# Optimization experiments

Hardware: AMD Instinct MI355X
Metric: run time of the kernel (lower is better)

The kernel has to match this reference:

```python
import jax, jax.numpy as jnp
import numpy as np

IN_SIZES = [64, 128, 256]
HIDDEN = [512, 512]
ENC = 256
COUNTS = [100000, 80000, 60000]


def _xavier(key, fan_in, fan_out):
    # xavier_uniform with gain('sigmoid') == 1
    lim = float(np.sqrt(6.0 / (fan_in + fan_out)))
    return jax.random.uniform(key, (fan_in, fan_out), jnp.float32, -lim, lim)


def setup_inputs() -> dict:
    key = jax.random.key(0)
    ks = jax.random.split(key, 32)
    inp = {}
    ki = 0
    for t, (n, d) in enumerate(zip(COUNTS, IN_SIZES)):
        inp[f"x{t}"] = jax.random.normal(ks[ki], (n, d), dtype=jnp.float32)
        ki += 1
    # node_type sorted by type, counts match x tensors (invariant of the module)
    inp["node_type"] = jnp.concatenate(
        [jnp.full((n,), t, dtype=jnp.int32) for t, n in enumerate(COUNTS)])
    for t, d_in in enumerate(IN_SIZES):
        sizes = [d_in] + HIDDEN + [ENC]
        for i in range(len(sizes) - 1):
            inp[f"W{t}_{i+1}"] = _xavier(ks[ki], sizes[i], sizes[i + 1])
            ki += 1
            inp[f"b{t}_{i+1}"] = jnp.zeros((sizes[i + 1],), jnp.float32)
    return inp


def _mlp(x, layers):
    # each layer is Linear followed by Sigmoid (including the last)
    for W, b in layers:
        x = jax.nn.sigmoid(x @ W + b)
    return x


def reference(x0, x1, x2, node_type,
              W0_1, b0_1, W0_2, b0_2, W0_3, b0_3,
              W1_1, b1_1, W1_2, b1_2, W1_3, b1_3,
              W2_1, b2_1, W2_2, b2_2, W2_3, b2_3):
    xs = [x0, x1, x2]
    params = [
        [(W0_1, b0_1), (W0_2, b0_2), (W0_3, b0_3)],
        [(W1_1, b1_1), (W1_2, b1_2), (W1_3, b1_3)],
        [(W2_1, b2_1), (W2_2, b2_2), (W2_3, b2_3)],
    ]
    N = node_type.shape[0]
    X = jnp.zeros((N, ENC), dtype=jnp.float32)
    for nt in range(len(xs)):
        # static per-type count -> fixed-size nonzero works under jit
        idx = jnp.nonzero(node_type == nt, size=xs[nt].shape[0])[0]
        X = X.at[idx].set(_mlp(xs[nt], params[nt]))
    return X
```

## Files before the change

### kernel.cpp

```cpp
#include <hip/hip_runtime.h>
#include <hip/hip_bf16.h>

typedef __bf16 bf16x8 __attribute__((ext_vector_type(8)));
typedef __bf16 bf16x4 __attribute__((ext_vector_type(4)));
typedef float  f32x16 __attribute__((ext_vector_type(16)));

#define BM 64
#define S  520
#define SF 260

struct PrepParams {
    const float* src[9];
    int Kt[9];
    int Mg[9];
    int N[9];
    int blkEnd[9];
    int unitBase[9];
};

__global__ void __launch_bounds__(256)
prep_weights(PrepParams p, uint4* __restrict__ dst) {
    __shared__ float tile[32][128];
    int b = blockIdx.x;
    int w = 0;
    while (b >= p.blkEnd[w]) ++w;
    int local = b - ((w == 0) ? 0 : p.blkEnd[w - 1]);
    int mgc = p.Mg[w];
    int kt = local / mgc;
    int mg = local - kt * mgc;
    const float* src = p.src[w];
    int N = p.N[w];
    int Kc = p.Kt[w] * 2;
    int t = threadIdx.x;

    int row0 = kt * 32, col0 = mg * 128;
#pragma unroll
    for (int i = 0; i < 4; ++i) {
        int e4 = t + i * 256;
        int r = e4 >> 5;
        int c4 = e4 & 31;
        float4 v = *(const float4*)&src[(size_t)(row0 + r) * N + col0 + c4 * 4];
        *(float4*)&tile[r][c4 * 4] = v;
    }
    __syncthreads();

#pragma unroll
    for (int rep = 0; rep < 2; ++rep) {
        int ul = t + rep * 256;
        int lane = ul & 63;
        int kcl = (ul >> 6) & 1;
        int mtl = ul >> 7;
        int gUnit = p.unitBase[w] +
                    ((mg * 4 + mtl) * Kc + (kt * 2 + kcl)) * 64 + lane;
        int lr = kcl * 16 + ((lane >> 5) << 3);
        int lc = mtl * 32 + (lane & 31);
        alignas(16) unsigned short u8[8];
#pragma unroll
        for (int j = 0; j < 8; ++j)
            u8[j] = __builtin_bit_cast(unsigned short, (__bf16)tile[lr + j][lc]);
        dst[gUnit] = *(const uint4*)u8;
    }
}

struct MlpParams {
    const float* X[3];
    const unsigned short* Wp[3];
    const float* B1[3];
    const float* B2[3];
    const float* B3[3];
    int dIn[3];
    int Nt[3];
    int rowOff[3];
    int blkStart[3];
};

__device__ __forceinline__ float sigmoidf(float z) {
    return __builtin_amdgcn_rcpf(
        1.0f + __builtin_amdgcn_exp2f(-1.442695040888963f * z));
}

template <int MT, bool TO_LDS>
__device__ __forceinline__ void layer(
    unsigned short* __restrict__ buf,
    const unsigned short* __restrict__ W,
    const float* __restrict__ bias,
    int K, int wave, int lane)
{
    const int Kc = K >> 4;
    const int half = lane >> 5;
    const int lr = lane & 31;

    f32x16 acc[2][MT];
#pragma unroll
    for (int n = 0; n < 2; ++n)
#pragma unroll
        for (int m = 0; m < MT; ++m)
#pragma unroll
            for (int e = 0; e < 16; ++e)
                acc[n][m][e] = 0.0f;

    const unsigned short* bp0 = buf + lr * S + half * 8;
    const unsigned short* bp1 = bp0 + 32 * S;
    const unsigned short* ap = W + (size_t)wave * MT * Kc * 512 + lane * 8;

    for (int kc = 0; kc < Kc; ++kc) {
        bf16x8 b0 = *(const bf16x8*)(bp0 + kc * 16);
        bf16x8 b1 = *(const bf16x8*)(bp1 + kc * 16);
#pragma unroll
        for (int m = 0; m < MT; ++m) {
            bf16x8 a = *(const bf16x8*)(ap + ((size_t)m * Kc + kc) * 512);
            acc[0][m] = __builtin_amdgcn_mfma_f32_32x32x16_bf16(
                a, b0, acc[0][m], 0, 0, 0);
            acc[1][m] = __builtin_amdgcn_mfma_f32_32x32x16_bf16(
                a, b1, acc[1][m], 0, 0, 0);
        }
    }

    __syncthreads();

#pragma unroll
    for (int m = 0; m < MT; ++m) {
        int mt = wave * MT + m;
#pragma unroll
        for (int g = 0; g < 4; ++g) {
            int f0 = mt * 32 + g * 8 + half * 4;
            float4 bv = *(const float4*)(bias + f0);
#pragma unroll
            for (int n = 0; n < 2; ++n) {
                int r = n * 32 + lr;
                float s0 = sigmoidf(acc[n][m][g * 4 + 0] + bv.x);
                float s1 = sigmoidf(acc[n][m][g * 4 + 1] + bv.y);
                float s2 = sigmoidf(acc[n][m][g * 4 + 2] + bv.z);
                float s3 = sigmoidf(acc[n][m][g * 4 + 3] + bv.w);
                if constexpr (TO_LDS) {
                    bf16x4 h = {(__bf16)s0, (__bf16)s1, (__bf16)s2, (__bf16)s3};
                    *(bf16x4*)(buf + r * S + f0) = h;
                } else {
                    float* fb = (float*)buf;
                    *(float4*)(fb + r * SF + f0) =
                        make_float4(s0, s1, s2, s3);
                }
            }
        }
    }
}

__global__ void __launch_bounds__(512, 4)
mlp_fused(MlpParams p, float* __restrict__ out) {
    extern __shared__ unsigned short buf[];

    int b = blockIdx.x;
    int t = (b >= p.blkStart[1]) + (b >= p.blkStart[2]);
    int blk = b - p.blkStart[t];
    int dIn = p.dIn[t];
    int Nt = p.Nt[t];
    int row0 = blk * BM;
    const float* X = p.X[t];
    const unsigned short* W1 = p.Wp[t];
    const unsigned short* W2 = W1 + dIn * 512;
    const unsigned short* W3 = W2 + 512 * 512;

    int tid = threadIdx.x;
    int wave = tid >> 6;
    int lane = tid & 63;

    int d4 = dIn >> 2;
    int s4 = 31 - __clz(d4);
    int nf4 = BM * d4;
    for (int i = tid; i < nf4; i += 512) {
        int r = i >> s4;
        int c4 = i & (d4 - 1);
        int grow = row0 + r;
        float4 v = make_float4(0.f, 0.f, 0.f, 0.f);
        if (grow < Nt) v = ((const float4*)X)[(size_t)grow * d4 + c4];
        ushort4 u;
        u.x = __builtin_bit_cast(unsigned short, (__bf16)v.x);
        u.y = __builtin_bit_cast(unsigned short, (__bf16)v.y);
        u.z = __builtin_bit_cast(unsigned short, (__bf16)v.z);
        u.w = __builtin_bit_cast(unsigned short, (__bf16)v.w);
        *(ushort4*)(buf + r * S + c4 * 4) = u;
    }
    __syncthreads();

    layer<2, true>(buf, W1, p.B1[t], dIn, wave, lane);
    __syncthreads();
    layer<2, true>(buf, W2, p.B2[t], 512, wave, lane);
    __syncthreads();
    layer<1, false>(buf, W3, p.B3[t], 512, wave, lane);
    __syncthreads();

    const float* fb = (const float*)buf;
    float* gOut = out + (size_t)(p.rowOff[t] + row0) * 256;
    for (int i = tid; i < BM * 64; i += 512) {
        int r = i >> 6;
        int c4 = i & 63;
        if (row0 + r < Nt)
            *(float4*)(gOut + r * 256 + c4 * 4) =
                *(const float4*)(fb + r * SF + c4 * 4);
    }
}

extern "C" void kernel_launch(void* const* d_in, const int* in_sizes, int n_in,
                              void* d_out, int out_size, void* d_ws, size_t ws_size,
                              hipStream_t stream) {
    const int IN0[3] = {64, 128, 256};
    const int CNT[3] = {100000, 80000, 60000};

    PrepParams pp;
    int blocks = 0, ubase = 0;
    for (int t = 0; t < 3; ++t) {
        int Ks[3] = {IN0[t], 512, 512};
        int Ns[3] = {512, 512, 256};
        for (int l = 0; l < 3; ++l) {
            int w = t * 3 + l;
            pp.src[w] = (const float*)d_in[4 + t * 6 + l * 2];
            pp.Kt[w] = Ks[l] >> 5;
            pp.Mg[w] = Ns[l] >> 7;
            pp.N[w] = Ns[l];
            pp.unitBase[w] = ubase;
            blocks += pp.Kt[w] * pp.Mg[w];
            pp.blkEnd[w] = blocks;
            ubase += (Ks[l] * Ns[l]) >> 3;
        }
    }
    prep_weights<<<dim3(blocks), dim3(256), 0, stream>>>(pp, (uint4*)d_ws);

    MlpParams mp;
    int woff = 0, roff = 0, boff = 0;
    for (int t = 0; t < 3; ++t) {
        mp.X[t] = (const float*)d_in[t];
        mp.Wp[t] = (const unsigned short*)d_ws + woff;
        mp.B1[t] = (const float*)d_in[4 + t * 6 + 1];
        mp.B2[t] = (const float*)d_in[4 + t * 6 + 3];
        mp.B3[t] = (const float*)d_in[4 + t * 6 + 5];
        mp.dIn[t] = IN0[t];
        mp.Nt[t] = CNT[t];
        mp.rowOff[t] = roff;
        mp.blkStart[t] = boff;
        woff += IN0[t] * 512 + 512 * 512 + 512 * 256;
        roff += CNT[t];
        boff += (CNT[t] + BM - 1) / BM;
    }
    size_t lds = (size_t)BM * S * sizeof(unsigned short);
    mlp_fused<<<dim3(boff), dim3(512), lds, stream>>>(mp, (float*)d_out);
}
```

Before: 645.4 us.

## Double row tile, prefetch weight fragments, specialize K, remap blocks across XCDs

Raises the rows per workgroup from 64 to 128, so each wave now computes four 32-row tiles and every weight fragment loaded from global memory feeds twice as many MFMAs. The K loop is made a compile-time constant per layer and fully unrolled, with a four-deep register ring that prefetches weight fragments ahead of use. Block IDs are remapped so that consecutive row tiles land on the same XCD, which should improve L2 reuse of weights. The cost is doubled LDS use per block and many more accumulator and prefetch registers, which lowers occupancy and risks register spills.

```diff
diff --git a/kernel.cpp b/kernel.cpp
--- a/kernel.cpp
+++ b/kernel.cpp
@@ -5,9 +5,10 @@
 typedef __bf16 bf16x4 __attribute__((ext_vector_type(4)));
 typedef float  f32x16 __attribute__((ext_vector_type(16)));
 
-#define BM 64
+#define BM 128
 #define S  520
 #define SF 260
+#define NT 4
 
 struct PrepParams {
     const float* src[9];
@@ -79,40 +80,52 @@
         1.0f + __builtin_amdgcn_exp2f(-1.442695040888963f * z));
 }
 
-template <int MT, bool TO_LDS>
+template <int KC, int MT, bool TO_LDS>
 __device__ __forceinline__ void layer(
     unsigned short* __restrict__ buf,
     const unsigned short* __restrict__ W,
     const float* __restrict__ bias,
-    int K, int wave, int lane)
+    int wave, int lane)
 {
-    const int Kc = K >> 4;
     const int half = lane >> 5;
     const int lr = lane & 31;
 
-    f32x16 acc[2][MT];
-#pragma unroll
-    for (int n = 0; n < 2; ++n)
+    f32x16 acc[NT][MT];
+#pragma unroll
+    for (int n = 0; n < NT; ++n)
 #pragma unroll
         for (int m = 0; m < MT; ++m)
 #pragma unroll
             for (int e = 0; e < 16; ++e)
                 acc[n][m][e] = 0.0f;
 
-    const unsigned short* bp0 = buf + lr * S + half * 8;
-    const unsigned short* bp1 = bp0 + 32 * S;
-    const unsigned short* ap = W + (size_t)wave * MT * Kc * 512 + lane * 8;
-
-    for (int kc = 0; kc < Kc; ++kc) {
-        bf16x8 b0 = *(const bf16x8*)(bp0 + kc * 16);
-        bf16x8 b1 = *(const bf16x8*)(bp1 + kc * 16);
-#pragma unroll
-        for (int m = 0; m < MT; ++m) {
-            bf16x8 a = *(const bf16x8*)(ap + ((size_t)m * Kc + kc) * 512);
-            acc[0][m] = __builtin_amdgcn_mfma_f32_32x32x16_bf16(
-                a, b0, acc[0][m], 0, 0, 0);
-            acc[1][m] = __builtin_amdgcn_mfma_f32_32x32x16_bf16(
-                a, b1, acc[1][m], 0, 0, 0);
+    const unsigned short* bp = buf + lr * S + half * 8;
+    const unsigned short* ap = W + (size_t)wave * MT * KC * 512 + lane * 8;
+
+    bf16x8 aPf[4][MT];
+#pragma unroll
+    for (int p = 0; p < 4; ++p)
+#pragma unroll
+        for (int m = 0; m < MT; ++m)
+            aPf[p][m] = *(const bf16x8*)(ap + ((size_t)m * KC + p) * 512);
+
+#pragma unroll
+    for (int kc = 0; kc < KC; ++kc) {
+        bf16x8 b[NT];
+#pragma unroll
+        for (int n = 0; n < NT; ++n)
+            b[n] = *(const bf16x8*)(bp + (size_t)n * 32 * S + kc * 16);
+#pragma unroll
+        for (int m = 0; m < MT; ++m)
+#pragma unroll
+            for (int n = 0; n < NT; ++n)
+                acc[n][m] = __builtin_amdgcn_mfma_f32_32x32x16_bf16(
+                    aPf[kc & 3][m], b[n], acc[n][m], 0, 0, 0);
+        if (kc + 4 < KC) {
+#pragma unroll
+            for (int m = 0; m < MT; ++m)
+                aPf[kc & 3][m] =
+                    *(const bf16x8*)(ap + ((size_t)m * KC + (kc + 4)) * 512);
         }
     }
 
@@ -126,7 +139,7 @@
             int f0 = mt * 32 + g * 8 + half * 4;
             float4 bv = *(const float4*)(bias + f0);
 #pragma unroll
-            for (int n = 0; n < 2; ++n) {
+            for (int n = 0; n < NT; ++n) {
                 int r = n * 32 + lr;
                 float s0 = sigmoidf(acc[n][m][g * 4 + 0] + bv.x);
                 float s1 = sigmoidf(acc[n][m][g * 4 + 1] + bv.y);
@@ -145,11 +158,16 @@
     }
 }
 
-__global__ void __launch_bounds__(512, 4)
+__global__ void __launch_bounds__(512, 2)
 mlp_fused(MlpParams p, float* __restrict__ out) {
     extern __shared__ unsigned short buf[];
 
-    int b = blockIdx.x;
+    int nwg = gridDim.x;
+    int bid = blockIdx.x;
+    int q = nwg >> 3, r8 = nwg & 7;
+    int xcd = bid & 7, lid = bid >> 3;
+    int b = (xcd < r8 ? xcd * (q + 1) : r8 * (q + 1) + (xcd - r8) * q) + lid;
+
     int t = (b >= p.blkStart[1]) + (b >= p.blkStart[2]);
     int blk = b - p.blkStart[t];
     int dIn = p.dIn[t];
@@ -182,11 +200,13 @@
     }
     __syncthreads();
 
-    layer<2, true>(buf, W1, p.B1[t], dIn, wave, lane);
-    __syncthreads();
-    layer<2, true>(buf, W2, p.B2[t], 512, wave, lane);
-    __syncthreads();
-    layer<1, false>(buf, W3, p.B3[t], 512, wave, lane);
+    if (t == 0)      layer< 4, 2, true>(buf, W1, p.B1[t], wave, lane);
+    else if (t == 1) layer< 8, 2, true>(buf, W1, p.B1[t], wave, lane);
+    else             layer<16, 2, true>(buf, W1, p.B1[t], wave, lane);
+    __syncthreads();
+    layer<32, 2, true>(buf, W2, p.B2[t], wave, lane);
+    __syncthreads();
+    layer<32, 1, false>(buf, W3, p.B3[t], wave, lane);
     __syncthreads();
 
     const float* fb = (const float*)buf;
```

After: 657.9 us. No clear change (+1.9%).

## Double-buffer weight panels in LDS via async global loads, remap waves and XCDs

Applied to the files above, without the earlier changes.

Weights are repacked k-major so each 32-wide k-step panel is contiguous, then staged into a double-buffered LDS panel with global_load_lds while the previous panel feeds MFMAs. Each wave now owns one 32-row batch tile and a set of feature tiles, instead of reading weights straight from global memory per wave. Block IDs are remapped so consecutive tiles land on the same XCD for L2 locality. The cost is a much larger LDS footprint (occupancy bound lowered to 2 blocks) and a barrier per k-step.

```diff
diff --git a/kernel.cpp b/kernel.cpp
--- a/kernel.cpp
+++ b/kernel.cpp
@@ -8,6 +8,7 @@
 #define BM 64
 #define S  520
 #define SF 260
+#define PANS 16384
 
 struct PrepParams {
     const float* src[9];
@@ -30,7 +31,7 @@
     int mg = local - kt * mgc;
     const float* src = p.src[w];
     int N = p.N[w];
-    int Kc = p.Kt[w] * 2;
+    int Nmt = N >> 5;
     int t = threadIdx.x;
 
     int row0 = kt * 32, col0 = mg * 128;
@@ -50,8 +51,8 @@
         int lane = ul & 63;
         int kcl = (ul >> 6) & 1;
         int mtl = ul >> 7;
-        int gUnit = p.unitBase[w] +
-                    ((mg * 4 + mtl) * Kc + (kt * 2 + kcl)) * 64 + lane;
+        int mt = mg * 4 + mtl;
+        int gUnit = p.unitBase[w] + ((kt * Nmt + mt) * 2 + kcl) * 64 + lane;
         int lr = kcl * 16 + ((lane >> 5) << 3);
         int lc = mtl * 32 + (lane & 31);
         alignas(16) unsigned short u8[8];
@@ -79,90 +80,120 @@
         1.0f + __builtin_amdgcn_exp2f(-1.442695040888963f * z));
 }
 
-template <int MT, bool TO_LDS>
+__device__ __forceinline__ void gload_lds16(const void* g, void* l) {
+    __builtin_amdgcn_global_load_lds(
+        (const __attribute__((address_space(1))) unsigned int*)g,
+        (__attribute__((address_space(3))) unsigned int*)l, 16, 0, 0);
+}
+
+template <int M>
+__device__ __forceinline__ void stageW(unsigned short* pan, int bufIdx,
+                                       const uint4* src, int wave, int lane) {
+    unsigned short* dst = pan + bufIdx * PANS + (wave * M) * 512;
+    const uint4* s = src + (size_t)(wave * M) * 64 + lane;
+#pragma unroll
+    for (int i = 0; i < M; ++i)
+        gload_lds16(s + i * 64, dst + i * 512);
+}
+
+template <int KSTEPS, int MTW, int NEXTM, bool TO_LDS>
 __device__ __forceinline__ void layer(
     unsigned short* __restrict__ buf,
-    const unsigned short* __restrict__ W,
+    unsigned short* __restrict__ pan,
+    const uint4* __restrict__ W,
+    const uint4* __restrict__ Wnext,
     const float* __restrict__ bias,
-    int K, int wave, int lane)
+    int wave, int lane, int& cur)
 {
-    const int Kc = K >> 4;
+    const int bt = wave >> 2;
+    const int fg = wave & 3;
     const int half = lane >> 5;
     const int lr = lane & 31;
 
-    f32x16 acc[2][MT];
-#pragma unroll
-    for (int n = 0; n < 2; ++n)
-#pragma unroll
-        for (int m = 0; m < MT; ++m)
-#pragma unroll
-            for (int e = 0; e < 16; ++e)
-                acc[n][m][e] = 0.0f;
-
-    const unsigned short* bp0 = buf + lr * S + half * 8;
-    const unsigned short* bp1 = bp0 + 32 * S;
-    const unsigned short* ap = W + (size_t)wave * MT * Kc * 512 + lane * 8;
-
-    for (int kc = 0; kc < Kc; ++kc) {
-        bf16x8 b0 = *(const bf16x8*)(bp0 + kc * 16);
-        bf16x8 b1 = *(const bf16x8*)(bp1 + kc * 16);
-#pragma unroll
-        for (int m = 0; m < MT; ++m) {
-            bf16x8 a = *(const bf16x8*)(ap + ((size_t)m * Kc + kc) * 512);
-            acc[0][m] = __builtin_amdgcn_mfma_f32_32x32x16_bf16(
-                a, b0, acc[0][m], 0, 0, 0);
-            acc[1][m] = __builtin_amdgcn_mfma_f32_32x32x16_bf16(
-                a, b1, acc[1][m], 0, 0, 0);
-        }
-    }
-
-    __syncthreads();
-
-#pragma unroll
-    for (int m = 0; m < MT; ++m) {
-        int mt = wave * MT + m;
+    f32x16 acc[MTW];
+#pragma unroll
+    for (int m = 0; m < MTW; ++m)
+#pragma unroll
+        for (int e = 0; e < 16; ++e)
+            acc[m][e] = 0.0f;
+
+    const unsigned short* bp = buf + (size_t)(bt * 32 + lr) * S + half * 8;
+
+#pragma unroll
+    for (int kc2 = 0; kc2 < KSTEPS; ++kc2) {
+        if (kc2 + 1 < KSTEPS) {
+            stageW<MTW>(pan, cur ^ 1,
+                        W + (size_t)(kc2 + 1) * (MTW * 512), wave, lane);
+        } else if constexpr (NEXTM > 0) {
+            stageW<NEXTM>(pan, cur ^ 1, Wnext, wave, lane);
+        }
+        const unsigned short* pcur = pan + cur * PANS;
+#pragma unroll
+        for (int kcl = 0; kcl < 2; ++kcl) {
+            bf16x8 b = *(const bf16x8*)(bp + (kc2 * 2 + kcl) * 16);
+#pragma unroll
+            for (int m = 0; m < MTW; ++m) {
+                bf16x8 a = *(const bf16x8*)(
+                    pcur + (((fg * MTW + m) * 2 + kcl) * 64 + lane) * 8);
+                acc[m] = __builtin_amdgcn_mfma_f32_32x32x16_bf16(
+                    a, b, acc[m], 0, 0, 0);
+            }
+        }
+        __syncthreads();
+        cur ^= 1;
+    }
+
+#pragma unroll
+    for (int m = 0; m < MTW; ++m) {
+        int mt = fg * MTW + m;
 #pragma unroll
         for (int g = 0; g < 4; ++g) {
             int f0 = mt * 32 + g * 8 + half * 4;
             float4 bv = *(const float4*)(bias + f0);
-#pragma unroll
-            for (int n = 0; n < 2; ++n) {
-                int r = n * 32 + lr;
-                float s0 = sigmoidf(acc[n][m][g * 4 + 0] + bv.x);
-                float s1 = sigmoidf(acc[n][m][g * 4 + 1] + bv.y);
-                float s2 = sigmoidf(acc[n][m][g * 4 + 2] + bv.z);
-                float s3 = sigmoidf(acc[n][m][g * 4 + 3] + bv.w);
-                if constexpr (TO_LDS) {
-                    bf16x4 h = {(__bf16)s0, (__bf16)s1, (__bf16)s2, (__bf16)s3};
-                    *(bf16x4*)(buf + r * S + f0) = h;
-                } else {
-                    float* fb = (float*)buf;
-                    *(float4*)(fb + r * SF + f0) =
-                        make_float4(s0, s1, s2, s3);
-                }
+            int r = bt * 32 + lr;
+            float s0 = sigmoidf(acc[m][g * 4 + 0] + bv.x);
+            float s1 = sigmoidf(acc[m][g * 4 + 1] + bv.y);
+            float s2 = sigmoidf(acc[m][g * 4 + 2] + bv.z);
+            float s3 = sigmoidf(acc[m][g * 4 + 3] + bv.w);
+            if constexpr (TO_LDS) {
+                bf16x4 h = {(__bf16)s0, (__bf16)s1, (__bf16)s2, (__bf16)s3};
+                *(bf16x4*)(buf + (size_t)r * S + f0) = h;
+            } else {
+                float* fb = (float*)buf;
+                *(float4*)(fb + (size_t)r * SF + f0) =
+                    make_float4(s0, s1, s2, s3);
             }
         }
     }
 }
 
-__global__ void __launch_bounds__(512, 4)
+__global__ void __launch_bounds__(512, 2)
 mlp_fused(MlpParams p, float* __restrict__ out) {
     extern __shared__ unsigned short buf[];
-
-    int b = blockIdx.x;
+    unsigned short* pan = buf + BM * S;
+
+    int nwg = gridDim.x;
+    int bid = blockIdx.x;
+    int q = nwg >> 3, r8 = nwg & 7;
+    int xcd = bid & 7, lid = bid >> 3;
+    int b = (xcd < r8 ? xcd * (q + 1) : r8 * (q + 1) + (xcd - r8) * q) + lid;
+
     int t = (b >= p.blkStart[1]) + (b >= p.blkStart[2]);
     int blk = b - p.blkStart[t];
     int dIn = p.dIn[t];
     int Nt = p.Nt[t];
     int row0 = blk * BM;
     const float* X = p.X[t];
-    const unsigned short* W1 = p.Wp[t];
-    const unsigned short* W2 = W1 + dIn * 512;
-    const unsigned short* W3 = W2 + 512 * 512;
+    const uint4* W1u = (const uint4*)p.Wp[t];
+    const uint4* W2u = W1u + ((size_t)dIn * 512 >> 3);
+    const uint4* W3u = W2u + ((size_t)512 * 512 >> 3);
 
     int tid = threadIdx.x;
     int wave = tid >> 6;
     int lane = tid & 63;
+    int cur = 0;
+
+    stageW<4>(pan, 0, W1u, wave, lane);
 
     int d4 = dIn >> 2;
     int s4 = 31 - __clz(d4);
@@ -182,11 +213,13 @@
     }
     __syncthreads();
 
-    layer<2, true>(buf, W1, p.B1[t], dIn, wave, lane);
-    __syncthreads();
-    layer<2, true>(buf, W2, p.B2[t], 512, wave, lane);
-    __syncthreads();
-    layer<1, false>(buf, W3, p.B3[t], 512, wave, lane);
+    if (t == 0)      layer<2, 4, 4, true>(buf, pan, W1u, W2u, p.B1[t], wave, lane, cur);
+    else if (t == 1) layer<4, 4, 4, true>(buf, pan, W1u, W2u, p.B1[t], wave, lane, cur);
+    else             layer<8, 4, 4, true>(buf, pan, W1u, W2u, p.B1[t], wave, lane, cur);
+    __syncthreads();
+    layer<16, 4, 2, true>(buf, pan, W2u, W3u, p.B2[t], wave, lane, cur);
+    __syncthreads();
+    layer<16, 2, 0, false>(buf, pan, W3u, nullptr, p.B3[t], wave, lane, cur);
     __syncthreads();
 
     const float* fb = (const float*)buf;
@@ -241,6 +274,6 @@
         roff += CNT[t];
         boff += (CNT[t] + BM - 1) / BM;
     }
-    size_t lds = (size_t)BM * S * sizeof(unsigned short);
+    size_t lds = (size_t)(BM * S + 2 * PANS) * sizeof(unsigned short);
     mlp_fused<<<dim3(boff), dim3(512), lds, stream>>>(mp, (float*)d_out);
 }
```

Result: slower. 804.7 us (+24.7%).

## Prefetch weight fragments four k-steps ahead and remap blocks across XCDs

Applied to the files above, without the earlier changes.

The GEMM inner loop now uses compile-time K and keeps a 4-deep register ring of weight (A) fragments, so global loads are issued several MFMA steps before they are used and their latency is hidden. Layer 1 is dispatched to a specialized instantiation per node type. Block indices are also remapped so that consecutive logical blocks land on the same XCD, which is meant to improve L2 reuse of each type's weights. The cost is higher register pressure from the prefetch buffers, which could hurt occupancy under the 512x4 launch bounds.

```diff
diff --git a/kernel.cpp b/kernel.cpp
--- a/kernel.cpp
+++ b/kernel.cpp
@@ -5,6 +5,7 @@
 typedef __bf16 bf16x4 __attribute__((ext_vector_type(4)));
 typedef float  f32x16 __attribute__((ext_vector_type(16)));
 
+#define MFMA __builtin_amdgcn_mfma_f32_32x32x16_bf16
 #define BM 64
 #define S  520
 #define SF 260
@@ -79,14 +80,13 @@
         1.0f + __builtin_amdgcn_exp2f(-1.442695040888963f * z));
 }
 
-template <int MT, bool TO_LDS>
-__device__ __forceinline__ void layer(
+template <int K16, int MT, bool TO_LDS>
+__device__ __forceinline__ void layerP(
     unsigned short* __restrict__ buf,
     const unsigned short* __restrict__ W,
     const float* __restrict__ bias,
-    int K, int wave, int lane)
+    int wave, int lane)
 {
-    const int Kc = K >> 4;
     const int half = lane >> 5;
     const int lr = lane & 31;
 
@@ -101,18 +101,44 @@
 
     const unsigned short* bp0 = buf + lr * S + half * 8;
     const unsigned short* bp1 = bp0 + 32 * S;
-    const unsigned short* ap = W + (size_t)wave * MT * Kc * 512 + lane * 8;
-
-    for (int kc = 0; kc < Kc; ++kc) {
-        bf16x8 b0 = *(const bf16x8*)(bp0 + kc * 16);
-        bf16x8 b1 = *(const bf16x8*)(bp1 + kc * 16);
+    const unsigned short* ap = W + (size_t)wave * MT * K16 * 512 + lane * 8;
+
+    bf16x8 aPf[4][MT];
+#pragma unroll
+    for (int d = 0; d < 4; ++d)
+#pragma unroll
+        for (int m = 0; m < MT; ++m)
+            aPf[d][m] = *(const bf16x8*)(ap + ((size_t)m * K16 + d) * 512);
+
+    for (int kb = 0; kb + 4 < K16; kb += 4) {
+#pragma unroll
+        for (int u = 0; u < 4; ++u) {
+            int k = kb + u;
+            bf16x8 b0 = *(const bf16x8*)(bp0 + k * 16);
+            bf16x8 b1 = *(const bf16x8*)(bp1 + k * 16);
+            bf16x8 a[MT];
+#pragma unroll
+            for (int m = 0; m < MT; ++m) a[m] = aPf[u][m];
+#pragma unroll
+            for (int m = 0; m < MT; ++m)
+                aPf[u][m] =
+                    *(const bf16x8*)(ap + ((size_t)m * K16 + k + 4) * 512);
+#pragma unroll
+            for (int m = 0; m < MT; ++m) {
+                acc[0][m] = MFMA(a[m], b0, acc[0][m], 0, 0, 0);
+                acc[1][m] = MFMA(a[m], b1, acc[1][m], 0, 0, 0);
+            }
+        }
+    }
+#pragma unroll
+    for (int u = 0; u < 4; ++u) {
+        int k = K16 - 4 + u;
+        bf16x8 b0 = *(const bf16x8*)(bp0 + k * 16);
+        bf16x8 b1 = *(const bf16x8*)(bp1 + k * 16);
 #pragma unroll
         for (int m = 0; m < MT; ++m) {
-            bf16x8 a = *(const bf16x8*)(ap + ((size_t)m * Kc + kc) * 512);
-            acc[0][m] = __builtin_amdgcn_mfma_f32_32x32x16_bf16(
-                a, b0, acc[0][m], 0, 0, 0);
-            acc[1][m] = __builtin_amdgcn_mfma_f32_32x32x16_bf16(
-                a, b1, acc[1][m], 0, 0, 0);
+            acc[0][m] = MFMA(aPf[u][m], b0, acc[0][m], 0, 0, 0);
+            acc[1][m] = MFMA(aPf[u][m], b1, acc[1][m], 0, 0, 0);
         }
     }
 
@@ -149,7 +175,12 @@
 mlp_fused(MlpParams p, float* __restrict__ out) {
     extern __shared__ unsigned short buf[];
 
-    int b = blockIdx.x;
+    int nwg = gridDim.x;
+    int bid = blockIdx.x;
+    int q = nwg >> 3, r8 = nwg & 7;
+    int xcd = bid & 7, lid = bid >> 3;
+    int b = (xcd < r8 ? xcd * (q + 1) : r8 * (q + 1) + (xcd - r8) * q) + lid;
+
     int t = (b >= p.blkStart[1]) + (b >= p.blkStart[2]);
     int blk = b - p.blkStart[t];
     int dIn = p.dIn[t];
@@ -182,11 +213,13 @@
     }
     __syncthreads();
 
-    layer<2, true>(buf, W1, p.B1[t], dIn, wave, lane);
-    __syncthreads();
-    layer<2, true>(buf, W2, p.B2[t], 512, wave, lane);
-    __syncthreads();
-    layer<1, false>(buf, W3, p.B3[t], 512, wave, lane);
+    if (t == 0)      layerP<4,  2, true>(buf, W1, p.B1[0], wave, lane);
+    else if (t == 1) layerP<8,  2, true>(buf, W1, p.B1[1], wave, lane);
+    else             layerP<16, 2, true>(buf, W1, p.B1[2], wave, lane);
+    __syncthreads();
+    layerP<32, 2, true>(buf, W2, p.B2[t], wave, lane);
+    __syncthreads();
+    layerP<32, 1, false>(buf, W3, p.B3[t], wave, lane);
     __syncthreads();
 
     const float* fb = (const float*)buf;
```

After: 659.0 us. 1.02x slower.
